# Performance work log

Hardware: AMD Instinct MI355X
Metric: run time of the kernel (lower is better)

## Reference

```python
import jax, jax.numpy as jnp
import numpy as np

N, EM, EW, L, S = 20000, 100000, 25000, 128, 6


def _mlp(x, W1, b1, W2, b2, g, beta):
    # Linear -> ReLU -> Linear -> LayerNorm
    h = jax.nn.relu(x @ W1 + b1) @ W2 + b2
    mu = jnp.mean(h, axis=-1, keepdims=True)
    var = jnp.mean((h - mu) ** 2, axis=-1, keepdims=True)
    return g * (h - mu) * jax.lax.rsqrt(var + 1e-5) + beta


def _scatter_mean(attr, recv, n):
    s = jax.ops.segment_sum(attr, recv, num_segments=n)
    c = jax.ops.segment_sum(jnp.ones((attr.shape[0], 1), attr.dtype), recv, num_segments=n)
    return s / jnp.maximum(c, 1.0)


def setup_inputs() -> dict:
    key = jax.random.key(0)
    ks = jax.random.split(key, 16)

    def w(k, shape, fan_in):
        return (jax.random.normal(k, shape, jnp.float32) / np.sqrt(fan_in).astype(np.float32))

    inp = {
        'x': jax.random.normal(ks[0], (N, L), jnp.float32),
        'mesh_edge_attr': jax.random.normal(ks[1], (EM, L), jnp.float32),
        'world_edge_attr': jax.random.normal(ks[2], (EW, L), jnp.float32),
        'mesh_edge_index': jax.random.randint(ks[3], (2, EM), 0, N),
        'world_edge_index': jax.random.randint(ks[4], (2, EW), 0, N),
    }
    i = 5
    for pre in ('me', 'we', 'nd'):
        inp[pre + '_W1'] = w(ks[i], (S, 3 * L, L), 3 * L); i += 1
        inp[pre + '_b1'] = jnp.zeros((S, L), jnp.float32)
        inp[pre + '_W2'] = w(ks[i], (S, L, L), L); i += 1
        inp[pre + '_b2'] = jnp.zeros((S, L), jnp.float32)
        inp[pre + '_g'] = jnp.ones((S, L), jnp.float32)
        inp[pre + '_beta'] = jnp.zeros((S, L), jnp.float32)
    return inp


def reference(x, mesh_edge_attr, world_edge_attr, mesh_edge_index, world_edge_index,
              me_W1, me_b1, me_W2, me_b2, me_g, me_beta,
              we_W1, we_b1, we_W2, we_b2, we_g, we_beta,
              nd_W1, nd_b1, nd_W2, nd_b2, nd_g, nd_beta):
    ms, mr = mesh_edge_index[0], mesh_edge_index[1]
    ws, wr = world_edge_index[0], world_edge_index[1]
    n = x.shape[0]

    def step(carry, p):
        x, mea, wea = carry
        (mW1, mb1, mW2, mb2, mg, mbe,
         wW1, wb1, wW2, wb2, wg, wbe,
         nW1, nb1, nW2, nb2, ng, nbe) = p
        # EdgeModel: gather + concat + MLP, residual into edge attrs
        mea = mea + _mlp(jnp.concatenate([x[ms], x[mr], mea], axis=-1), mW1, mb1, mW2, mb2, mg, mbe)
        wea = wea + _mlp(jnp.concatenate([x[ws], x[wr], wea], axis=-1), wW1, wb1, wW2, wb2, wg, wbe)
        # NodeModel: scatter-mean over both edge sets + concat + MLP, residual
        agg = jnp.concatenate([x, _scatter_mean(mea, mr, n), _scatter_mean(wea, wr, n)], axis=-1)
        x = x + _mlp(agg, nW1, nb1, nW2, nb2, ng, nbe)
        return (x, mea, wea), None

    params = (me_W1, me_b1, me_W2, me_b2, me_g, me_beta,
              we_W1, we_b1, we_W2, we_b2, we_g, we_beta,
              nd_W1, nd_b1, nd_W2, nd_b2, nd_g, nd_beta)
    (x, mea, wea), _ = jax.lax.scan(step, (x, mesh_edge_attr, world_edge_attr), params)
    return x, mea, wea
```

## Files before the change

kernel.cpp:

```cpp
#include <hip/hip_runtime.h>

constexpr int LDIM  = 128;
constexpr int NNODE = 20000;
constexpr int EM_N  = 100000;
constexpr int EW_N  = 25000;
constexpr int NSTEP = 6;

typedef short bf16x8 __attribute__((ext_vector_type(8)));
typedef float f32x4  __attribute__((ext_vector_type(4)));

struct MlpParams {
  const float* x;
  const float* attrIn;
  float*       attrOut;
  const int*   src;
  const int*   dst;
  float*       sum1;
  float*       sum2;
  const float* inv1;
  const float* inv2;
  const short* W1H;
  const short* W1L;
  const short* W2H;
  const short* W2L;
  const float* b1;
  const float* b2;
  const float* gam;
  const float* bet;
  int nRows;
};

__device__ __forceinline__ short f2b(float f) {
  unsigned int u = __float_as_uint(f);
  u = (u + 0x7fffu + ((u >> 16) & 1u)) >> 16;
  return (short)u;
}
__device__ __forceinline__ float b2f(short s) {
  return __uint_as_float(((unsigned int)(unsigned short)s) << 16);
}

template<bool IS_EDGE>
__launch_bounds__(256, 2)
__global__ void mlp_kernel(MlpParams pmA, MlpParams pmB, int blocksA) {
  const bool isA = (int)blockIdx.x < blocksA;
  const MlpParams P = isA ? pmA : pmB;
  const int bid  = isA ? (int)blockIdx.x : (int)blockIdx.x - blocksA;
  const int row0 = bid * 128;

  __shared__ __align__(16) short Abuf[128][40];
  __shared__ __align__(16) short Bhi[128][40];
  __shared__ __align__(16) short Blo[128][40];
  __shared__ __align__(16) short Hbuf[128][136];
  __shared__ float b1s[128], b2s[128], gs[128], bes[128];
  __shared__ int   idxa[128], idxb[128];
  __shared__ float inv1s[128], inv2s[128];
  __shared__ float sumL[2][128], sqL[2][128];
  __shared__ float muL[128], rsL[128];

  const int t = threadIdx.x;

  if (t < 128) {
    b1s[t] = P.b1[t];
    gs[t]  = P.gam[t];
    if (IS_EDGE) {
      int r = row0 + t;
      idxa[t] = (r < P.nRows) ? P.src[r] : 0;
    } else {
      int r = min(row0 + t, P.nRows - 1);
      inv1s[t] = P.inv1[r];
    }
  } else {
    int t2 = t - 128;
    b2s[t2] = P.b2[t2];
    bes[t2] = P.bet[t2];
    if (IS_EDGE) {
      int r = row0 + t2;
      idxb[t2] = (r < P.nRows) ? P.dst[r] : 0;
    } else {
      int r = min(row0 + t2, P.nRows - 1);
      inv2s[t2] = P.inv2[r];
    }
  }

  const int l   = t & 63;
  const int wid = t >> 6;
  const int wr  = wid >> 1, wcc = wid & 1;
  const int lr  = l & 15,  lg  = l >> 4;

  const int  srow  = t >> 1, sh = t & 1;
  const int  sgRow = row0 + srow;
  const bool sval  = sgRow < P.nRows;

  f32x4 acc[4][4];
#pragma unroll
  for (int i = 0; i < 4; ++i)
#pragma unroll
    for (int j = 0; j < 4; ++j) acc[i][j] = f32x4{0.f, 0.f, 0.f, 0.f};

  for (int kc = 0; kc < 12; ++kc) {
    __syncthreads();
    {
      const int seg = kc >> 2, part = kc & 3;
      float v[16];
      if (sval) {
        const float* sbase;
        float sc = 1.0f;
        if (IS_EDGE) {
          sbase = (seg == 0) ? P.x + (size_t)idxa[srow] * LDIM
                : (seg == 1) ? P.x + (size_t)idxb[srow] * LDIM
                             : P.attrIn + (size_t)sgRow * LDIM;
        } else {
          if (seg == 0)      { sbase = P.x    + (size_t)sgRow * LDIM; }
          else if (seg == 1) { sbase = P.sum1 + (size_t)sgRow * LDIM; sc = inv1s[srow]; }
          else               { sbase = P.sum2 + (size_t)sgRow * LDIM; sc = inv2s[srow]; }
        }
        const float4* s4 = (const float4*)(sbase + part * 32 + sh * 16);
        float4 a0 = s4[0], a1 = s4[1], a2 = s4[2], a3 = s4[3];
        v[0]=a0.x;  v[1]=a0.y;  v[2]=a0.z;  v[3]=a0.w;
        v[4]=a1.x;  v[5]=a1.y;  v[6]=a1.z;  v[7]=a1.w;
        v[8]=a2.x;  v[9]=a2.y;  v[10]=a2.z; v[11]=a2.w;
        v[12]=a3.x; v[13]=a3.y; v[14]=a3.z; v[15]=a3.w;
        if (!IS_EDGE && seg != 0) {
#pragma unroll
          for (int e = 0; e < 16; ++e) v[e] *= sc;
          float4 z = {0.f, 0.f, 0.f, 0.f};
          float4* zp = (float4*)(sbase + part * 32 + sh * 16);
          zp[0] = z; zp[1] = z; zp[2] = z; zp[3] = z;
        }
      } else {
#pragma unroll
        for (int e = 0; e < 16; ++e) v[e] = 0.f;
      }
      bf16x8 o0, o1;
#pragma unroll
      for (int e = 0; e < 8; ++e) { o0[e] = f2b(v[e]); o1[e] = f2b(v[8 + e]); }
      *(bf16x8*)&Abuf[srow][sh * 16]     = o0;
      *(bf16x8*)&Abuf[srow][sh * 16 + 8] = o1;
    }
    {
      const size_t off = (size_t)srow * 384 + kc * 32 + sh * 16;
      const short* wh = P.W1H + off;
      const short* wl = P.W1L + off;
      *(bf16x8*)&Bhi[srow][sh * 16]     = *(const bf16x8*)wh;
      *(bf16x8*)&Bhi[srow][sh * 16 + 8] = *(const bf16x8*)(wh + 8);
      *(bf16x8*)&Blo[srow][sh * 16]     = *(const bf16x8*)wl;
      *(bf16x8*)&Blo[srow][sh * 16 + 8] = *(const bf16x8*)(wl + 8);
    }
    __syncthreads();
    bf16x8 av[4], bh[4], bl[4];
#pragma unroll
    for (int rt = 0; rt < 4; ++rt) av[rt] = *(const bf16x8*)&Abuf[wr * 64 + rt * 16 + lr][lg * 8];
#pragma unroll
    for (int ct = 0; ct < 4; ++ct) {
      bh[ct] = *(const bf16x8*)&Bhi[wcc * 64 + ct * 16 + lr][lg * 8];
      bl[ct] = *(const bf16x8*)&Blo[wcc * 64 + ct * 16 + lr][lg * 8];
    }
#pragma unroll
    for (int rt = 0; rt < 4; ++rt)
#pragma unroll
      for (int ct = 0; ct < 4; ++ct) {
        acc[rt][ct] = __builtin_amdgcn_mfma_f32_16x16x32_bf16(av[rt], bl[ct], acc[rt][ct], 0, 0, 0);
        acc[rt][ct] = __builtin_amdgcn_mfma_f32_16x16x32_bf16(av[rt], bh[ct], acc[rt][ct], 0, 0, 0);
      }
  }

#pragma unroll
  for (int rt = 0; rt < 4; ++rt)
#pragma unroll
    for (int ct = 0; ct < 4; ++ct) {
      const int cc = wcc * 64 + ct * 16 + lr;
      const float bb = b1s[cc];
#pragma unroll
      for (int q = 0; q < 4; ++q) {
        const int rr = wr * 64 + rt * 16 + lg * 4 + q;
        Hbuf[rr][cc] = f2b(fmaxf(acc[rt][ct][q] + bb, 0.f));
      }
    }

  f32x4 acc2[4][4];
#pragma unroll
  for (int i = 0; i < 4; ++i)
#pragma unroll
    for (int j = 0; j < 4; ++j) acc2[i][j] = f32x4{0.f, 0.f, 0.f, 0.f};

  for (int kc = 0; kc < 4; ++kc) {
    __syncthreads();
    {
      const size_t off = (size_t)srow * 128 + kc * 32 + sh * 16;
      const short* wh = P.W2H + off;
      const short* wl = P.W2L + off;
      *(bf16x8*)&Bhi[srow][sh * 16]     = *(const bf16x8*)wh;
      *(bf16x8*)&Bhi[srow][sh * 16 + 8] = *(const bf16x8*)(wh + 8);
      *(bf16x8*)&Blo[srow][sh * 16]     = *(const bf16x8*)wl;
      *(bf16x8*)&Blo[srow][sh * 16 + 8] = *(const bf16x8*)(wl + 8);
    }
    __syncthreads();
    bf16x8 av2[4], bh2[4], bl2[4];
#pragma unroll
    for (int rt = 0; rt < 4; ++rt) av2[rt] = *(const bf16x8*)&Hbuf[wr * 64 + rt * 16 + lr][kc * 32 + lg * 8];
#pragma unroll
    for (int ct = 0; ct < 4; ++ct) {
      bh2[ct] = *(const bf16x8*)&Bhi[wcc * 64 + ct * 16 + lr][lg * 8];
      bl2[ct] = *(const bf16x8*)&Blo[wcc * 64 + ct * 16 + lr][lg * 8];
    }
#pragma unroll
    for (int rt = 0; rt < 4; ++rt)
#pragma unroll
      for (int ct = 0; ct < 4; ++ct) {
        acc2[rt][ct] = __builtin_amdgcn_mfma_f32_16x16x32_bf16(av2[rt], bl2[ct], acc2[rt][ct], 0, 0, 0);
        acc2[rt][ct] = __builtin_amdgcn_mfma_f32_16x16x32_bf16(av2[rt], bh2[ct], acc2[rt][ct], 0, 0, 0);
      }
  }

  float s1[4][4], s2[4][4];
#pragma unroll
  for (int rt = 0; rt < 4; ++rt)
#pragma unroll
    for (int q = 0; q < 4; ++q) { s1[rt][q] = 0.f; s2[rt][q] = 0.f; }
#pragma unroll
  for (int rt = 0; rt < 4; ++rt)
#pragma unroll
    for (int ct = 0; ct < 4; ++ct) {
      const float bb = b2s[wcc * 64 + ct * 16 + lr];
#pragma unroll
      for (int q = 0; q < 4; ++q) {
        float v = acc2[rt][ct][q] + bb;
        acc2[rt][ct][q] = v;
        s1[rt][q] += v;
        s2[rt][q] += v * v;
      }
    }
#pragma unroll
  for (int m = 1; m < 16; m <<= 1) {
#pragma unroll
    for (int rt = 0; rt < 4; ++rt)
#pragma unroll
      for (int q = 0; q < 4; ++q) {
        s1[rt][q] += __shfl_xor(s1[rt][q], m);
        s2[rt][q] += __shfl_xor(s2[rt][q], m);
      }
  }
  __syncthreads();
  {
    const int rt = lr >> 2, q = lr & 3;
    const int rr = wr * 64 + rt * 16 + lg * 4 + q;
    sumL[wcc][rr] = s1[rt][q];
    sqL[wcc][rr]  = s2[rt][q];
  }
  __syncthreads();
  if (t < 128) {
    const float tot = sumL[0][t] + sumL[1][t];
    const float tsq = sqL[0][t] + sqL[1][t];
    const float mu  = tot * (1.0f / 128.0f);
    const float var = tsq * (1.0f / 128.0f) - mu * mu;
    muL[t] = mu;
    rsL[t] = rsqrtf(var + 1e-5f);
  }
  __syncthreads();

#pragma unroll
  for (int rt = 0; rt < 4; ++rt) {
#pragma unroll
    for (int q = 0; q < 4; ++q) {
      const int rr = wr * 64 + rt * 16 + lg * 4 + q;
      const int grow = row0 + rr;
      if (grow < P.nRows) {
        const float mu = muL[rr], rs = rsL[rr];
        const float* rin = P.attrIn + (size_t)grow * LDIM;
        float* rout = P.attrOut + (size_t)grow * LDIM;
        float* ssum = nullptr;
        if (IS_EDGE) ssum = P.sum1 + (size_t)idxb[rr] * LDIM;
#pragma unroll
        for (int ct = 0; ct < 4; ++ct) {
          const int cc = wcc * 64 + ct * 16 + lr;
          const float o = gs[cc] * (acc2[rt][ct][q] - mu) * rs + bes[cc] + rin[cc];
          rout[cc] = o;
          if (IS_EDGE) atomicAdd(ssum + cc, o);
        }
      }
    }
  }
}

__global__ void prep_weights(const float* w1a, const float* w1b, const float* w1c,
                             const float* w2a, const float* w2b, const float* w2c,
                             short* w1h, short* w1l, short* w2h, short* w2l) {
  int i = blockIdx.x * 256 + threadIdx.x;
  constexpr int N1 = 18 * 128 * 384;
  constexpr int N2 = 18 * 128 * 128;
  if (i < N1) {
    int g = i / (128 * 384);
    int rem = i - g * (128 * 384);
    int n = rem / 384, k = rem - n * 384;
    int m = g / 6, s = g - m * 6;
    const float* src = (m == 0) ? w1a : (m == 1) ? w1b : w1c;
    float f = src[(size_t)s * (384 * 128) + (size_t)k * 128 + n];
    short hi = f2b(f);
    w1h[i] = hi;
    w1l[i] = f2b(f - b2f(hi));
  } else if (i < N1 + N2) {
    int j = i - N1;
    int g = j / (128 * 128);
    int rem = j - g * (128 * 128);
    int n = rem / 128, k = rem - n * 128;
    int m = g / 6, s = g - m * 6;
    const float* src = (m == 0) ? w2a : (m == 1) ? w2b : w2c;
    float f = src[(size_t)s * (128 * 128) + (size_t)k * 128 + n];
    short hi = f2b(f);
    w2h[j] = hi;
    w2l[j] = f2b(f - b2f(hi));
  }
}

__global__ void prep_deg(const int* mr, const int* wrcv, int* degm, int* degw) {
  int i = blockIdx.x * 256 + threadIdx.x;
  if (i < EM_N) atomicAdd(&degm[mr[i]], 1);
  else if (i < EM_N + EW_N) atomicAdd(&degw[wrcv[i - EM_N]], 1);
}

__global__ void prep_inv(const int* degm, const int* degw, float* invm, float* invw) {
  int i = blockIdx.x * 256 + threadIdx.x;
  if (i < NNODE) {
    invm[i] = 1.0f / fmaxf((float)degm[i], 1.0f);
    invw[i] = 1.0f / fmaxf((float)degw[i], 1.0f);
  }
}

extern "C" void kernel_launch(void* const* d_in, const int* in_sizes, int n_in,
                              void* d_out, int out_size, void* d_ws, size_t ws_size,
                              hipStream_t stream) {
  (void)in_sizes; (void)n_in; (void)out_size; (void)ws_size;
  const float* x_in   = (const float*)d_in[0];
  const float* mea_in = (const float*)d_in[1];
  const float* wea_in = (const float*)d_in[2];
  const int*   mei    = (const int*)d_in[3];
  const int*   wei    = (const int*)d_in[4];
  const float* W1s[3] = { (const float*)d_in[5],  (const float*)d_in[11], (const float*)d_in[17] };
  const float* B1s[3] = { (const float*)d_in[6],  (const float*)d_in[12], (const float*)d_in[18] };
  const float* W2s[3] = { (const float*)d_in[7],  (const float*)d_in[13], (const float*)d_in[19] };
  const float* B2s[3] = { (const float*)d_in[8],  (const float*)d_in[14], (const float*)d_in[20] };
  const float* Gs[3]  = { (const float*)d_in[9],  (const float*)d_in[15], (const float*)d_in[21] };
  const float* Be[3]  = { (const float*)d_in[10], (const float*)d_in[16], (const float*)d_in[22] };

  float* xo  = (float*)d_out;
  float* meo = xo  + (size_t)NNODE * LDIM;
  float* weo = meo + (size_t)EM_N * LDIM;

  float* msum = (float*)d_ws;
  float* wsum = msum + (size_t)NNODE * LDIM;
  int*   degm = (int*)(wsum + (size_t)NNODE * LDIM);
  int*   degw = degm + NNODE;
  float* invm = (float*)(degw + NNODE);
  float* invw = invm + NNODE;
  short* w1h  = (short*)(invw + NNODE);
  short* w1l  = w1h + (size_t)18 * 128 * 384;
  short* w2h  = w1l + (size_t)18 * 128 * 384;
  short* w2l  = w2h + (size_t)18 * 128 * 128;

  size_t zbytes = (size_t)2 * NNODE * LDIM * 4 + (size_t)2 * NNODE * 4;
  hipMemsetAsync(d_ws, 0, zbytes, stream);

  {
    int tot = 18 * 128 * 384 + 18 * 128 * 128;
    prep_weights<<<dim3((tot + 255) / 256), 256, 0, stream>>>(
        W1s[0], W1s[1], W1s[2], W2s[0], W2s[1], W2s[2], w1h, w1l, w2h, w2l);
  }
  prep_deg<<<dim3((EM_N + EW_N + 255) / 256), 256, 0, stream>>>(mei + EM_N, wei + EW_N, degm, degw);
  prep_inv<<<dim3((NNODE + 255) / 256), 256, 0, stream>>>(degm, degw, invm, invw);

  const int MB = (EM_N + 127) / 128;
  const int WB = (EW_N + 127) / 128;
  const int NB = (NNODE + 127) / 128;

  const float* xc = x_in;
  const float* mc = mea_in;
  const float* wc = wea_in;

  for (int s = 0; s < NSTEP; ++s) {
    MlpParams pm{}, pw{}, pn{};

    pm.x = xc; pm.attrIn = mc; pm.attrOut = meo;
    pm.src = mei; pm.dst = mei + EM_N;
    pm.sum1 = msum; pm.sum2 = nullptr; pm.inv1 = nullptr; pm.inv2 = nullptr;
    pm.W1H = w1h + (size_t)(0 * 6 + s) * 128 * 384;
    pm.W1L = w1l + (size_t)(0 * 6 + s) * 128 * 384;
    pm.W2H = w2h + (size_t)(0 * 6 + s) * 128 * 128;
    pm.W2L = w2l + (size_t)(0 * 6 + s) * 128 * 128;
    pm.b1 = B1s[0] + s * LDIM; pm.b2 = B2s[0] + s * LDIM;
    pm.gam = Gs[0] + s * LDIM; pm.bet = Be[0] + s * LDIM;
    pm.nRows = EM_N;

    pw.x = xc; pw.attrIn = wc; pw.attrOut = weo;
    pw.src = wei; pw.dst = wei + EW_N;
    pw.sum1 = wsum; pw.sum2 = nullptr; pw.inv1 = nullptr; pw.inv2 = nullptr;
    pw.W1H = w1h + (size_t)(1 * 6 + s) * 128 * 384;
    pw.W1L = w1l + (size_t)(1 * 6 + s) * 128 * 384;
    pw.W2H = w2h + (size_t)(1 * 6 + s) * 128 * 128;
    pw.W2L = w2l + (size_t)(1 * 6 + s) * 128 * 128;
    pw.b1 = B1s[1] + s * LDIM; pw.b2 = B2s[1] + s * LDIM;
    pw.gam = Gs[1] + s * LDIM; pw.bet = Be[1] + s * LDIM;
    pw.nRows = EW_N;

    mlp_kernel<true><<<dim3(MB + WB), 256, 0, stream>>>(pm, pw, MB);

    pn.x = xc; pn.attrIn = xc; pn.attrOut = xo;
    pn.src = nullptr; pn.dst = nullptr;
    pn.sum1 = msum; pn.sum2 = wsum; pn.inv1 = invm; pn.inv2 = invw;
    pn.W1H = w1h + (size_t)(2 * 6 + s) * 128 * 384;
    pn.W1L = w1l + (size_t)(2 * 6 + s) * 128 * 384;
    pn.W2H = w2h + (size_t)(2 * 6 + s) * 128 * 128;
    pn.W2L = w2l + (size_t)(2 * 6 + s) * 128 * 128;
    pn.b1 = B1s[2] + s * LDIM; pn.b2 = B2s[2] + s * LDIM;
    pn.gam = Gs[2] + s * LDIM; pn.bet = Be[2] + s * LDIM;
    pn.nRows = NNODE;

    mlp_kernel<false><<<dim3(NB), 256, 0, stream>>>(pn, pn, NB);

    xc = xo; mc = meo; wc = weo;
  }
}
```

Baseline: 946.2 us.

## Double-buffer activations, read weights from global directly, retile node MLP to 32-row blocks

Restructures the MLP kernel. The activation tile is now double-buffered so the next chunk's global loads overlap with the current MFMAs, which cuts one barrier per k-step. Weight fragments are read straight from global/L2 into registers instead of staged through shared memory. The second GEMM is computed transposed so that epilogue stores become float4. The kernel is templated on block rows so the node pass uses 32-row blocks, giving more blocks and higher occupancy, and launch bounds are raised. The cost is more global weight traffic per wave, and the changed occupancy may increase register pressure.

```diff
diff --git a/kernel.cpp b/kernel.cpp
--- a/kernel.cpp
+++ b/kernel.cpp
@@ -7,6 +7,7 @@
 constexpr int NSTEP = 6;
 
 typedef short bf16x8 __attribute__((ext_vector_type(8)));
+typedef short bf16x4 __attribute__((ext_vector_type(4)));
 typedef float f32x4  __attribute__((ext_vector_type(4)));
 
 struct MlpParams {
@@ -39,218 +40,248 @@
   return __uint_as_float(((unsigned int)(unsigned short)s) << 16);
 }
 
-template<bool IS_EDGE>
-__launch_bounds__(256, 2)
+template<int BR, bool IS_EDGE>
+__launch_bounds__(256, (BR == 128) ? 3 : 4)
 __global__ void mlp_kernel(MlpParams pmA, MlpParams pmB, int blocksA) {
+  constexpr int WC    = (BR == 128) ? 2 : 4;
+  constexpr int WR    = 4 / WC;
+  constexpr int WROWS = BR / WR;
+  constexpr int WCOLS = 128 / WC;
+  constexpr int MREP  = WROWS / 16;
+  constexpr int NREP  = WCOLS / 16;
+  constexpr int TPR   = 256 / BR;
+  constexpr int FPT   = 32 / TPR;
+  constexpr int NV4   = FPT / 4;
+
   const bool isA = (int)blockIdx.x < blocksA;
   const MlpParams P = isA ? pmA : pmB;
   const int bid  = isA ? (int)blockIdx.x : (int)blockIdx.x - blocksA;
-  const int row0 = bid * 128;
-
-  __shared__ __align__(16) short Abuf[128][40];
-  __shared__ __align__(16) short Bhi[128][40];
-  __shared__ __align__(16) short Blo[128][40];
-  __shared__ __align__(16) short Hbuf[128][136];
+  const int row0 = bid * BR;
+
+  __shared__ __align__(16) short Abuf[2][BR][40];
+  __shared__ __align__(16) short Hbuf[BR][40];
   __shared__ float b1s[128], b2s[128], gs[128], bes[128];
-  __shared__ int   idxa[128], idxb[128];
-  __shared__ float inv1s[128], inv2s[128];
-  __shared__ float sumL[2][128], sqL[2][128];
-  __shared__ float muL[128], rsL[128];
+  __shared__ int   idxa[BR], idxb[BR];
+  __shared__ float inv1s[BR], inv2s[BR];
+  __shared__ float sumL[WC][BR], sqL[WC][BR], muL[BR], rsL[BR];
 
   const int t = threadIdx.x;
 
-  if (t < 128) {
-    b1s[t] = P.b1[t];
-    gs[t]  = P.gam[t];
+  if (t < 128) { b1s[t] = P.b1[t]; gs[t] = P.gam[t]; }
+  else         { b2s[t - 128] = P.b2[t - 128]; bes[t - 128] = P.bet[t - 128]; }
+  if (t < BR) {
     if (IS_EDGE) {
       int r = row0 + t;
       idxa[t] = (r < P.nRows) ? P.src[r] : 0;
+      idxb[t] = (r < P.nRows) ? P.dst[r] : 0;
     } else {
       int r = min(row0 + t, P.nRows - 1);
       inv1s[t] = P.inv1[r];
-    }
-  } else {
-    int t2 = t - 128;
-    b2s[t2] = P.b2[t2];
-    bes[t2] = P.bet[t2];
-    if (IS_EDGE) {
-      int r = row0 + t2;
-      idxb[t2] = (r < P.nRows) ? P.dst[r] : 0;
-    } else {
-      int r = min(row0 + t2, P.nRows - 1);
-      inv2s[t2] = P.inv2[r];
-    }
-  }
+      inv2s[t] = P.inv2[r];
+    }
+  }
+  __syncthreads();
 
   const int l   = t & 63;
   const int wid = t >> 6;
-  const int wr  = wid >> 1, wcc = wid & 1;
+  const int wr  = wid / WC, wcc = wid % WC;
   const int lr  = l & 15,  lg  = l >> 4;
 
-  const int  srow  = t >> 1, sh = t & 1;
+  const int  srow  = t / TPR, sh = t % TPR;
   const int  sgRow = row0 + srow;
   const bool sval  = sgRow < P.nRows;
 
-  f32x4 acc[4][4];
-#pragma unroll
-  for (int i = 0; i < 4; ++i)
-#pragma unroll
-    for (int j = 0; j < 4; ++j) acc[i][j] = f32x4{0.f, 0.f, 0.f, 0.f};
-
+  int gA = 0, gB = 0; float sc1 = 1.f, sc2 = 1.f;
+  if (IS_EDGE) { gA = idxa[srow]; gB = idxb[srow]; }
+  else         { sc1 = inv1s[srow]; sc2 = inv2s[srow]; }
+
+  auto loadChunk = [&](int kc, float* v) {
+    const int seg = kc >> 2, part = kc & 3;
+    if (sval) {
+      const float* sbase; float sc = 1.f;
+      if (IS_EDGE) {
+        sbase = (seg == 0) ? P.x + (size_t)gA * LDIM
+              : (seg == 1) ? P.x + (size_t)gB * LDIM
+                           : P.attrIn + (size_t)sgRow * LDIM;
+      } else {
+        if (seg == 0)      { sbase = P.x    + (size_t)sgRow * LDIM; }
+        else if (seg == 1) { sbase = P.sum1 + (size_t)sgRow * LDIM; sc = sc1; }
+        else               { sbase = P.sum2 + (size_t)sgRow * LDIM; sc = sc2; }
+      }
+      const float4* s4 = (const float4*)(sbase + part * 32 + sh * FPT);
+#pragma unroll
+      for (int c = 0; c < NV4; ++c) {
+        float4 a = s4[c];
+        v[c * 4 + 0] = a.x; v[c * 4 + 1] = a.y; v[c * 4 + 2] = a.z; v[c * 4 + 3] = a.w;
+      }
+      if (!IS_EDGE && seg != 0) {
+#pragma unroll
+        for (int e = 0; e < FPT; ++e) v[e] *= sc;
+        float4 z = {0.f, 0.f, 0.f, 0.f};
+        float4* zp = (float4*)(sbase + part * 32 + sh * FPT);
+#pragma unroll
+        for (int c = 0; c < NV4; ++c) zp[c] = z;
+      }
+    } else {
+#pragma unroll
+      for (int e = 0; e < FPT; ++e) v[e] = 0.f;
+    }
+  };
+
+  auto storeChunk = [&](int buf, const float* v) {
+    if constexpr (FPT == 16) {
+      bf16x8 o0, o1;
+#pragma unroll
+      for (int e = 0; e < 8; ++e) { o0[e] = f2b(v[e]); o1[e] = f2b(v[8 + e]); }
+      *(bf16x8*)&Abuf[buf][srow][sh * 16]     = o0;
+      *(bf16x8*)&Abuf[buf][srow][sh * 16 + 8] = o1;
+    } else {
+      bf16x4 o;
+#pragma unroll
+      for (int e = 0; e < 4; ++e) o[e] = f2b(v[e]);
+      *(bf16x4*)&Abuf[buf][srow][sh * 4] = o;
+    }
+  };
+
+  f32x4 acc[MREP][NREP];
+#pragma unroll
+  for (int i = 0; i < MREP; ++i)
+#pragma unroll
+    for (int j = 0; j < NREP; ++j) acc[i][j] = f32x4{0.f, 0.f, 0.f, 0.f};
+
+  {
+    float v0[FPT];
+    loadChunk(0, v0);
+    storeChunk(0, v0);
+  }
+  __syncthreads();
+
+  const short* w1hB = P.W1H + (size_t)(wcc * WCOLS + lr) * 384 + lg * 8;
+  const short* w1lB = P.W1L + (size_t)(wcc * WCOLS + lr) * 384 + lg * 8;
+
+#pragma unroll
   for (int kc = 0; kc < 12; ++kc) {
+    float vnext[FPT];
+    if (kc < 11) loadChunk(kc + 1, vnext);
+    bf16x8 bh[NREP], bl[NREP];
+#pragma unroll
+    for (int ni = 0; ni < NREP; ++ni) {
+      bh[ni] = *(const bf16x8*)(w1hB + (size_t)ni * (16 * 384) + kc * 32);
+      bl[ni] = *(const bf16x8*)(w1lB + (size_t)ni * (16 * 384) + kc * 32);
+    }
+    bf16x8 av[MREP];
+#pragma unroll
+    for (int mi = 0; mi < MREP; ++mi)
+      av[mi] = *(const bf16x8*)&Abuf[kc & 1][wr * WROWS + mi * 16 + lr][lg * 8];
+#pragma unroll
+    for (int mi = 0; mi < MREP; ++mi)
+#pragma unroll
+      for (int ni = 0; ni < NREP; ++ni) {
+        acc[mi][ni] = __builtin_amdgcn_mfma_f32_16x16x32_bf16(av[mi], bl[ni], acc[mi][ni], 0, 0, 0);
+        acc[mi][ni] = __builtin_amdgcn_mfma_f32_16x16x32_bf16(av[mi], bh[ni], acc[mi][ni], 0, 0, 0);
+      }
+    if (kc < 11) storeChunk((kc + 1) & 1, vnext);
     __syncthreads();
-    {
-      const int seg = kc >> 2, part = kc & 3;
-      float v[16];
-      if (sval) {
-        const float* sbase;
-        float sc = 1.0f;
-        if (IS_EDGE) {
-          sbase = (seg == 0) ? P.x + (size_t)idxa[srow] * LDIM
-                : (seg == 1) ? P.x + (size_t)idxb[srow] * LDIM
-                             : P.attrIn + (size_t)sgRow * LDIM;
-        } else {
-          if (seg == 0)      { sbase = P.x    + (size_t)sgRow * LDIM; }
-          else if (seg == 1) { sbase = P.sum1 + (size_t)sgRow * LDIM; sc = inv1s[srow]; }
-          else               { sbase = P.sum2 + (size_t)sgRow * LDIM; sc = inv2s[srow]; }
+  }
+
+  unsigned int hpk[MREP][NREP][2];
+#pragma unroll
+  for (int ni = 0; ni < NREP; ++ni) {
+    const float bb = b1s[wcc * WCOLS + ni * 16 + lr];
+#pragma unroll
+    for (int mi = 0; mi < MREP; ++mi)
+#pragma unroll
+      for (int qp = 0; qp < 2; ++qp) {
+        unsigned int lo = (unsigned short)f2b(fmaxf(acc[mi][ni][2 * qp]     + bb, 0.f));
+        unsigned int hi = (unsigned short)f2b(fmaxf(acc[mi][ni][2 * qp + 1] + bb, 0.f));
+        hpk[mi][ni][qp] = lo | (hi << 16);
+      }
+  }
+
+  f32x4 acc2[NREP][MREP];
+#pragma unroll
+  for (int i = 0; i < NREP; ++i)
+#pragma unroll
+    for (int j = 0; j < MREP; ++j) acc2[i][j] = f32x4{0.f, 0.f, 0.f, 0.f};
+
+  const short* w2hB = P.W2H + (size_t)(wcc * WCOLS + lr) * 128 + lg * 8;
+  const short* w2lB = P.W2L + (size_t)(wcc * WCOLS + lr) * 128 + lg * 8;
+
+#pragma unroll
+  for (int kc = 0; kc < 4; ++kc) {
+    const int owner = (kc * 32) / WCOLS;
+    const int nib   = ((kc * 32) % WCOLS) / 16;
+    __syncthreads();
+    if (wcc == owner) {
+#pragma unroll
+      for (int mi = 0; mi < MREP; ++mi)
+#pragma unroll
+        for (int nio = 0; nio < 2; ++nio) {
+          const int ni = nib + nio;
+          const int cl = nio * 16 + lr;
+#pragma unroll
+          for (int qp = 0; qp < 2; ++qp) {
+            const int r = wr * WROWS + mi * 16 + lg * 4 + 2 * qp;
+            const unsigned int pk = hpk[mi][ni][qp];
+            Hbuf[r][cl]     = (short)(pk & 0xffffu);
+            Hbuf[r + 1][cl] = (short)(pk >> 16);
+          }
         }
-        const float4* s4 = (const float4*)(sbase + part * 32 + sh * 16);
-        float4 a0 = s4[0], a1 = s4[1], a2 = s4[2], a3 = s4[3];
-        v[0]=a0.x;  v[1]=a0.y;  v[2]=a0.z;  v[3]=a0.w;
-        v[4]=a1.x;  v[5]=a1.y;  v[6]=a1.z;  v[7]=a1.w;
-        v[8]=a2.x;  v[9]=a2.y;  v[10]=a2.z; v[11]=a2.w;
-        v[12]=a3.x; v[13]=a3.y; v[14]=a3.z; v[15]=a3.w;
-        if (!IS_EDGE && seg != 0) {
-#pragma unroll
-          for (int e = 0; e < 16; ++e) v[e] *= sc;
-          float4 z = {0.f, 0.f, 0.f, 0.f};
-          float4* zp = (float4*)(sbase + part * 32 + sh * 16);
-          zp[0] = z; zp[1] = z; zp[2] = z; zp[3] = z;
-        }
-      } else {
-#pragma unroll
-        for (int e = 0; e < 16; ++e) v[e] = 0.f;
-      }
-      bf16x8 o0, o1;
-#pragma unroll
-      for (int e = 0; e < 8; ++e) { o0[e] = f2b(v[e]); o1[e] = f2b(v[8 + e]); }
-      *(bf16x8*)&Abuf[srow][sh * 16]     = o0;
-      *(bf16x8*)&Abuf[srow][sh * 16 + 8] = o1;
-    }
-    {
-      const size_t off = (size_t)srow * 384 + kc * 32 + sh * 16;
-      const short* wh = P.W1H + off;
-      const short* wl = P.W1L + off;
-      *(bf16x8*)&Bhi[srow][sh * 16]     = *(const bf16x8*)wh;
-      *(bf16x8*)&Bhi[srow][sh * 16 + 8] = *(const bf16x8*)(wh + 8);
-      *(bf16x8*)&Blo[srow][sh * 16]     = *(const bf16x8*)wl;
-      *(bf16x8*)&Blo[srow][sh * 16 + 8] = *(const bf16x8*)(wl + 8);
     }
     __syncthreads();
-    bf16x8 av[4], bh[4], bl[4];
-#pragma unroll
-    for (int rt = 0; rt < 4; ++rt) av[rt] = *(const bf16x8*)&Abuf[wr * 64 + rt * 16 + lr][lg * 8];
-#pragma unroll
-    for (int ct = 0; ct < 4; ++ct) {
-      bh[ct] = *(const bf16x8*)&Bhi[wcc * 64 + ct * 16 + lr][lg * 8];
-      bl[ct] = *(const bf16x8*)&Blo[wcc * 64 + ct * 16 + lr][lg * 8];
-    }
-#pragma unroll
-    for (int rt = 0; rt < 4; ++rt)
-#pragma unroll
-      for (int ct = 0; ct < 4; ++ct) {
-        acc[rt][ct] = __builtin_amdgcn_mfma_f32_16x16x32_bf16(av[rt], bl[ct], acc[rt][ct], 0, 0, 0);
-        acc[rt][ct] = __builtin_amdgcn_mfma_f32_16x16x32_bf16(av[rt], bh[ct], acc[rt][ct], 0, 0, 0);
-      }
-  }
-
-#pragma unroll
-  for (int rt = 0; rt < 4; ++rt)
-#pragma unroll
-    for (int ct = 0; ct < 4; ++ct) {
-      const int cc = wcc * 64 + ct * 16 + lr;
-      const float bb = b1s[cc];
-#pragma unroll
-      for (int q = 0; q < 4; ++q) {
-        const int rr = wr * 64 + rt * 16 + lg * 4 + q;
-        Hbuf[rr][cc] = f2b(fmaxf(acc[rt][ct][q] + bb, 0.f));
-      }
-    }
-
-  f32x4 acc2[4][4];
-#pragma unroll
-  for (int i = 0; i < 4; ++i)
-#pragma unroll
-    for (int j = 0; j < 4; ++j) acc2[i][j] = f32x4{0.f, 0.f, 0.f, 0.f};
-
-  for (int kc = 0; kc < 4; ++kc) {
-    __syncthreads();
-    {
-      const size_t off = (size_t)srow * 128 + kc * 32 + sh * 16;
-      const short* wh = P.W2H + off;
-      const short* wl = P.W2L + off;
-      *(bf16x8*)&Bhi[srow][sh * 16]     = *(const bf16x8*)wh;
-      *(bf16x8*)&Bhi[srow][sh * 16 + 8] = *(const bf16x8*)(wh + 8);
-      *(bf16x8*)&Blo[srow][sh * 16]     = *(const bf16x8*)wl;
-      *(bf16x8*)&Blo[srow][sh * 16 + 8] = *(const bf16x8*)(wl + 8);
-    }
-    __syncthreads();
-    bf16x8 av2[4], bh2[4], bl2[4];
-#pragma unroll
-    for (int rt = 0; rt < 4; ++rt) av2[rt] = *(const bf16x8*)&Hbuf[wr * 64 + rt * 16 + lr][kc * 32 + lg * 8];
-#pragma unroll
-    for (int ct = 0; ct < 4; ++ct) {
-      bh2[ct] = *(const bf16x8*)&Bhi[wcc * 64 + ct * 16 + lr][lg * 8];
-      bl2[ct] = *(const bf16x8*)&Blo[wcc * 64 + ct * 16 + lr][lg * 8];
-    }
-#pragma unroll
-    for (int rt = 0; rt < 4; ++rt)
-#pragma unroll
-      for (int ct = 0; ct < 4; ++ct) {
-        acc2[rt][ct] = __builtin_amdgcn_mfma_f32_16x16x32_bf16(av2[rt], bl2[ct], acc2[rt][ct], 0, 0, 0);
-        acc2[rt][ct] = __builtin_amdgcn_mfma_f32_16x16x32_bf16(av2[rt], bh2[ct], acc2[rt][ct], 0, 0, 0);
-      }
-  }
-
-  float s1[4][4], s2[4][4];
-#pragma unroll
-  for (int rt = 0; rt < 4; ++rt)
-#pragma unroll
-    for (int q = 0; q < 4; ++q) { s1[rt][q] = 0.f; s2[rt][q] = 0.f; }
-#pragma unroll
-  for (int rt = 0; rt < 4; ++rt)
-#pragma unroll
-    for (int ct = 0; ct < 4; ++ct) {
-      const float bb = b2s[wcc * 64 + ct * 16 + lr];
-#pragma unroll
-      for (int q = 0; q < 4; ++q) {
-        float v = acc2[rt][ct][q] + bb;
-        acc2[rt][ct][q] = v;
-        s1[rt][q] += v;
-        s2[rt][q] += v * v;
-      }
-    }
-#pragma unroll
-  for (int m = 1; m < 16; m <<= 1) {
-#pragma unroll
-    for (int rt = 0; rt < 4; ++rt)
-#pragma unroll
-      for (int q = 0; q < 4; ++q) {
-        s1[rt][q] += __shfl_xor(s1[rt][q], m);
-        s2[rt][q] += __shfl_xor(s2[rt][q], m);
-      }
+    bf16x8 hv[MREP];
+#pragma unroll
+    for (int mi = 0; mi < MREP; ++mi)
+      hv[mi] = *(const bf16x8*)&Hbuf[wr * WROWS + mi * 16 + lr][lg * 8];
+    bf16x8 wh[NREP], wl[NREP];
+#pragma unroll
+    for (int ct = 0; ct < NREP; ++ct) {
+      wh[ct] = *(const bf16x8*)(w2hB + (size_t)ct * (16 * 128) + kc * 32);
+      wl[ct] = *(const bf16x8*)(w2lB + (size_t)ct * (16 * 128) + kc * 32);
+    }
+#pragma unroll
+    for (int ct = 0; ct < NREP; ++ct)
+#pragma unroll
+      for (int mi = 0; mi < MREP; ++mi) {
+        acc2[ct][mi] = __builtin_amdgcn_mfma_f32_16x16x32_bf16(wl[ct], hv[mi], acc2[ct][mi], 0, 0, 0);
+        acc2[ct][mi] = __builtin_amdgcn_mfma_f32_16x16x32_bf16(wh[ct], hv[mi], acc2[ct][mi], 0, 0, 0);
+      }
+  }
+
+  float s1[MREP], s2[MREP];
+#pragma unroll
+  for (int mi = 0; mi < MREP; ++mi) { s1[mi] = 0.f; s2[mi] = 0.f; }
+#pragma unroll
+  for (int ct = 0; ct < NREP; ++ct) {
+    const int n0 = wcc * WCOLS + ct * 16 + lg * 4;
+#pragma unroll
+    for (int q = 0; q < 4; ++q) {
+      const float bb = b2s[n0 + q];
+#pragma unroll
+      for (int mi = 0; mi < MREP; ++mi) {
+        const float v = acc2[ct][mi][q] + bb;
+        acc2[ct][mi][q] = v;
+        s1[mi] += v; s2[mi] += v * v;
+      }
+    }
+  }
+#pragma unroll
+  for (int mi = 0; mi < MREP; ++mi) {
+    s1[mi] += __shfl_xor(s1[mi], 16); s1[mi] += __shfl_xor(s1[mi], 32);
+    s2[mi] += __shfl_xor(s2[mi], 16); s2[mi] += __shfl_xor(s2[mi], 32);
+  }
+  if (lg == 0) {
+#pragma unroll
+    for (int mi = 0; mi < MREP; ++mi) {
+      sumL[wcc][wr * WROWS + mi * 16 + lr] = s1[mi];
+      sqL[wcc][wr * WROWS + mi * 16 + lr]  = s2[mi];
+    }
   }
   __syncthreads();
-  {
-    const int rt = lr >> 2, q = lr & 3;
-    const int rr = wr * 64 + rt * 16 + lg * 4 + q;
-    sumL[wcc][rr] = s1[rt][q];
-    sqL[wcc][rr]  = s2[rt][q];
-  }
-  __syncthreads();
-  if (t < 128) {
-    const float tot = sumL[0][t] + sumL[1][t];
-    const float tsq = sqL[0][t] + sqL[1][t];
+  if (t < BR) {
+    float tot = 0.f, tsq = 0.f;
+#pragma unroll
+    for (int w = 0; w < WC; ++w) { tot += sumL[w][t]; tsq += sqL[w][t]; }
     const float mu  = tot * (1.0f / 128.0f);
     const float var = tsq * (1.0f / 128.0f) - mu * mu;
     muL[t] = mu;
@@ -258,24 +289,39 @@
   }
   __syncthreads();
 
-#pragma unroll
-  for (int rt = 0; rt < 4; ++rt) {
-#pragma unroll
-    for (int q = 0; q < 4; ++q) {
-      const int rr = wr * 64 + rt * 16 + lg * 4 + q;
-      const int grow = row0 + rr;
-      if (grow < P.nRows) {
-        const float mu = muL[rr], rs = rsL[rr];
-        const float* rin = P.attrIn + (size_t)grow * LDIM;
-        float* rout = P.attrOut + (size_t)grow * LDIM;
-        float* ssum = nullptr;
-        if (IS_EDGE) ssum = P.sum1 + (size_t)idxb[rr] * LDIM;
-#pragma unroll
-        for (int ct = 0; ct < 4; ++ct) {
-          const int cc = wcc * 64 + ct * 16 + lr;
-          const float o = gs[cc] * (acc2[rt][ct][q] - mu) * rs + bes[cc] + rin[cc];
-          rout[cc] = o;
-          if (IS_EDGE) atomicAdd(ssum + cc, o);
+  float garr[NREP][4], bearr[NREP][4];
+#pragma unroll
+  for (int ct = 0; ct < NREP; ++ct) {
+    const int n0 = wcc * WCOLS + ct * 16 + lg * 4;
+#pragma unroll
+    for (int q = 0; q < 4; ++q) { garr[ct][q] = gs[n0 + q]; bearr[ct][q] = bes[n0 + q]; }
+  }
+
+#pragma unroll
+  for (int mi = 0; mi < MREP; ++mi) {
+    const int rl   = wr * WROWS + mi * 16 + lr;
+    const int grow = row0 + rl;
+    if (grow < P.nRows) {
+      const float mu = muL[rl], rs = rsL[rl];
+      const float* rin  = P.attrIn  + (size_t)grow * LDIM;
+      float*       rout = P.attrOut + (size_t)grow * LDIM;
+      float* ssum = nullptr;
+      if (IS_EDGE) ssum = P.sum1 + (size_t)idxb[rl] * LDIM;
+#pragma unroll
+      for (int ct = 0; ct < NREP; ++ct) {
+        const int n0 = wcc * WCOLS + ct * 16 + lg * 4;
+        const float4 old = *(const float4*)(rin + n0);
+        float4 oo;
+        oo.x = garr[ct][0] * (acc2[ct][mi][0] - mu) * rs + bearr[ct][0] + old.x;
+        oo.y = garr[ct][1] * (acc2[ct][mi][1] - mu) * rs + bearr[ct][1] + old.y;
+        oo.z = garr[ct][2] * (acc2[ct][mi][2] - mu) * rs + bearr[ct][2] + old.z;
+        oo.w = garr[ct][3] * (acc2[ct][mi][3] - mu) * rs + bearr[ct][3] + old.w;
+        *(float4*)(rout + n0) = oo;
+        if (IS_EDGE) {
+          atomicAdd(ssum + n0 + 0, oo.x);
+          atomicAdd(ssum + n0 + 1, oo.y);
+          atomicAdd(ssum + n0 + 2, oo.z);
+          atomicAdd(ssum + n0 + 3, oo.w);
         }
       }
     }
@@ -370,7 +416,7 @@
 
   const int MB = (EM_N + 127) / 128;
   const int WB = (EW_N + 127) / 128;
-  const int NB = (NNODE + 127) / 128;
+  const int NB = NNODE / 32;
 
   const float* xc = x_in;
   const float* mc = mea_in;
@@ -381,7 +427,7 @@
 
     pm.x = xc; pm.attrIn = mc; pm.attrOut = meo;
     pm.src = mei; pm.dst = mei + EM_N;
-    pm.sum1 = msum; pm.sum2 = nullptr; pm.inv1 = nullptr; pm.inv2 = nullptr;
+    pm.sum1 = msum;
     pm.W1H = w1h + (size_t)(0 * 6 + s) * 128 * 384;
     pm.W1L = w1l + (size_t)(0 * 6 + s) * 128 * 384;
     pm.W2H = w2h + (size_t)(0 * 6 + s) * 128 * 128;
@@ -392,7 +438,7 @@
 
     pw.x = xc; pw.attrIn = wc; pw.attrOut = weo;
     pw.src = wei; pw.dst = wei + EW_N;
-    pw.sum1 = wsum; pw.sum2 = nullptr; pw.inv1 = nullptr; pw.inv2 = nullptr;
+    pw.sum1 = wsum;
     pw.W1H = w1h + (size_t)(1 * 6 + s) * 128 * 384;
     pw.W1L = w1l + (size_t)(1 * 6 + s) * 128 * 384;
     pw.W2H = w2h + (size_t)(1 * 6 + s) * 128 * 128;
@@ -401,10 +447,9 @@
     pw.gam = Gs[1] + s * LDIM; pw.bet = Be[1] + s * LDIM;
     pw.nRows = EW_N;
 
-    mlp_kernel<true><<<dim3(MB + WB), 256, 0, stream>>>(pm, pw, MB);
+    mlp_kernel<128, true><<<dim3(MB + WB), 256, 0, stream>>>(pm, pw, MB);
 
     pn.x = xc; pn.attrIn = xc; pn.attrOut = xo;
-    pn.src = nullptr; pn.dst = nullptr;
     pn.sum1 = msum; pn.sum2 = wsum; pn.inv1 = invm; pn.inv2 = invw;
     pn.W1H = w1h + (size_t)(2 * 6 + s) * 128 * 384;
     pn.W1L = w1l + (size_t)(2 * 6 + s) * 128 * 384;
@@ -414,7 +459,7 @@
     pn.gam = Gs[2] + s * LDIM; pn.bet = Be[2] + s * LDIM;
     pn.nRows = NNODE;
 
-    mlp_kernel<false><<<dim3(NB), 256, 0, stream>>>(pn, pn, NB);
+    mlp_kernel<32, false><<<dim3(NB), 256, 0, stream>>>(pn, pn, NB);
 
     xc = xo; mc = meo; wc = weo;
   }
```

Result: slower. 1.892 ms (median of 2 runs) (+100.0%).

## Drop W1 low-part split and register-prefetch next K-chunk in MLP GEMMs

Applied to the files above, without the earlier changes.

The first-layer GEMM now uses a single bf16 copy of W1 instead of the hi/lo split, which halves its MFMA count and its weight traffic. Both GEMM loops now load the next K-chunk of activations and weights into registers while the current chunk is being computed, so global load latency overlaps the MFMAs. Activation address and scale computation is hoisted out of the loop, and invalid rows are masked by a zero multiplier. The cost is lower precision in the first layer, which may loosen accuracy against the fp32 reference, plus higher register pressure from the prefetch buffers.

```diff
diff --git a/kernel.cpp b/kernel.cpp
--- a/kernel.cpp
+++ b/kernel.cpp
@@ -7,6 +7,7 @@
 constexpr int NSTEP = 6;
 
 typedef short bf16x8 __attribute__((ext_vector_type(8)));
+typedef short bf16x4 __attribute__((ext_vector_type(4)));
 typedef float f32x4  __attribute__((ext_vector_type(4)));
 
 struct MlpParams {
@@ -20,7 +21,6 @@
   const float* inv1;
   const float* inv2;
   const short* W1H;
-  const short* W1L;
   const short* W2H;
   const short* W2L;
   const float* b1;
@@ -37,6 +37,12 @@
 }
 __device__ __forceinline__ float b2f(short s) {
   return __uint_as_float(((unsigned int)(unsigned short)s) << 16);
+}
+__device__ __forceinline__ bf16x4 cvt4(float4 a, float sc) {
+  bf16x4 o;
+  o[0] = f2b(a.x * sc); o[1] = f2b(a.y * sc);
+  o[2] = f2b(a.z * sc); o[3] = f2b(a.w * sc);
+  return o;
 }
 
 template<bool IS_EDGE>
@@ -81,6 +87,7 @@
       inv2s[t2] = P.inv2[r];
     }
   }
+  __syncthreads();
 
   const int l   = t & 63;
   const int wid = t >> 6;
@@ -90,6 +97,25 @@
   const int  srow  = t >> 1, sh = t & 1;
   const int  sgRow = row0 + srow;
   const bool sval  = sgRow < P.nRows;
+  const int  sgC   = sval ? sgRow : 0;
+  const float vmask = sval ? 1.f : 0.f;
+
+  const float* base0; const float* base1; const float* base2;
+  float sc1v = vmask, sc2v = vmask;
+  if (IS_EDGE) {
+    base0 = P.x + (size_t)idxa[srow] * LDIM + sh * 16;
+    base1 = P.x + (size_t)idxb[srow] * LDIM + sh * 16;
+    base2 = P.attrIn + (size_t)sgC * LDIM + sh * 16;
+  } else {
+    base0 = P.x    + (size_t)sgC * LDIM + sh * 16;
+    base1 = P.sum1 + (size_t)sgC * LDIM + sh * 16;
+    base2 = P.sum2 + (size_t)sgC * LDIM + sh * 16;
+    sc1v = inv1s[srow] * vmask;
+    sc2v = inv2s[srow] * vmask;
+  }
+
+  const int wrow = t >> 1, wsh = t & 1;
+  const short* w1base = P.W1H + (size_t)wrow * 384 + wsh * 16;
 
   f32x4 acc[4][4];
 #pragma unroll
@@ -97,71 +123,55 @@
 #pragma unroll
     for (int j = 0; j < 4; ++j) acc[i][j] = f32x4{0.f, 0.f, 0.f, 0.f};
 
+  float4 pA0, pA1, pA2, pA3;
+  bf16x8 pW0, pW1;
+  {
+    const float4* bp = (const float4*)base0;
+    pA0 = bp[0]; pA1 = bp[1]; pA2 = bp[2]; pA3 = bp[3];
+    pW0 = *(const bf16x8*)w1base;
+    pW1 = *(const bf16x8*)(w1base + 8);
+  }
+
+#pragma unroll
   for (int kc = 0; kc < 12; ++kc) {
-    __syncthreads();
+    const int seg = kc >> 2, part = kc & 3;
+    if (kc > 0) __syncthreads();
     {
-      const int seg = kc >> 2, part = kc & 3;
-      float v[16];
-      if (sval) {
-        const float* sbase;
-        float sc = 1.0f;
-        if (IS_EDGE) {
-          sbase = (seg == 0) ? P.x + (size_t)idxa[srow] * LDIM
-                : (seg == 1) ? P.x + (size_t)idxb[srow] * LDIM
-                             : P.attrIn + (size_t)sgRow * LDIM;
-        } else {
-          if (seg == 0)      { sbase = P.x    + (size_t)sgRow * LDIM; }
-          else if (seg == 1) { sbase = P.sum1 + (size_t)sgRow * LDIM; sc = inv1s[srow]; }
-          else               { sbase = P.sum2 + (size_t)sgRow * LDIM; sc = inv2s[srow]; }
-        }
-        const float4* s4 = (const float4*)(sbase + part * 32 + sh * 16);
-        float4 a0 = s4[0], a1 = s4[1], a2 = s4[2], a3 = s4[3];
-        v[0]=a0.x;  v[1]=a0.y;  v[2]=a0.z;  v[3]=a0.w;
-        v[4]=a1.x;  v[5]=a1.y;  v[6]=a1.z;  v[7]=a1.w;
-        v[8]=a2.x;  v[9]=a2.y;  v[10]=a2.z; v[11]=a2.w;
-        v[12]=a3.x; v[13]=a3.y; v[14]=a3.z; v[15]=a3.w;
-        if (!IS_EDGE && seg != 0) {
-#pragma unroll
-          for (int e = 0; e < 16; ++e) v[e] *= sc;
+      const float scK = (seg == 0) ? vmask : (seg == 1) ? sc1v : sc2v;
+      *(bf16x4*)&Abuf[srow][sh * 16 + 0]  = cvt4(pA0, scK);
+      *(bf16x4*)&Abuf[srow][sh * 16 + 4]  = cvt4(pA1, scK);
+      *(bf16x4*)&Abuf[srow][sh * 16 + 8]  = cvt4(pA2, scK);
+      *(bf16x4*)&Abuf[srow][sh * 16 + 12] = cvt4(pA3, scK);
+      *(bf16x8*)&Bhi[wrow][wsh * 16]     = pW0;
+      *(bf16x8*)&Bhi[wrow][wsh * 16 + 8] = pW1;
+      if constexpr (!IS_EDGE) {
+        if (seg != 0 && sval) {
           float4 z = {0.f, 0.f, 0.f, 0.f};
-          float4* zp = (float4*)(sbase + part * 32 + sh * 16);
+          float4* zp = (float4*)((seg == 1 ? base1 : base2) + part * 32);
           zp[0] = z; zp[1] = z; zp[2] = z; zp[3] = z;
         }
-      } else {
-#pragma unroll
-        for (int e = 0; e < 16; ++e) v[e] = 0.f;
-      }
-      bf16x8 o0, o1;
-#pragma unroll
-      for (int e = 0; e < 8; ++e) { o0[e] = f2b(v[e]); o1[e] = f2b(v[8 + e]); }
-      *(bf16x8*)&Abuf[srow][sh * 16]     = o0;
-      *(bf16x8*)&Abuf[srow][sh * 16 + 8] = o1;
-    }
-    {
-      const size_t off = (size_t)srow * 384 + kc * 32 + sh * 16;
-      const short* wh = P.W1H + off;
-      const short* wl = P.W1L + off;
-      *(bf16x8*)&Bhi[srow][sh * 16]     = *(const bf16x8*)wh;
-      *(bf16x8*)&Bhi[srow][sh * 16 + 8] = *(const bf16x8*)(wh + 8);
-      *(bf16x8*)&Blo[srow][sh * 16]     = *(const bf16x8*)wl;
-      *(bf16x8*)&Blo[srow][sh * 16 + 8] = *(const bf16x8*)(wl + 8);
+      }
     }
     __syncthreads();
-    bf16x8 av[4], bh[4], bl[4];
-#pragma unroll
-    for (int rt = 0; rt < 4; ++rt) av[rt] = *(const bf16x8*)&Abuf[wr * 64 + rt * 16 + lr][lg * 8];
-#pragma unroll
-    for (int ct = 0; ct < 4; ++ct) {
-      bh[ct] = *(const bf16x8*)&Bhi[wcc * 64 + ct * 16 + lr][lg * 8];
-      bl[ct] = *(const bf16x8*)&Blo[wcc * 64 + ct * 16 + lr][lg * 8];
-    }
-#pragma unroll
-    for (int rt = 0; rt < 4; ++rt)
-#pragma unroll
-      for (int ct = 0; ct < 4; ++ct) {
-        acc[rt][ct] = __builtin_amdgcn_mfma_f32_16x16x32_bf16(av[rt], bl[ct], acc[rt][ct], 0, 0, 0);
-        acc[rt][ct] = __builtin_amdgcn_mfma_f32_16x16x32_bf16(av[rt], bh[ct], acc[rt][ct], 0, 0, 0);
-      }
+    if (kc < 11) {
+      const int kn = kc + 1, segn = kn >> 2, partn = kn & 3;
+      const float4* bp = (const float4*)((segn == 0 ? base0 : segn == 1 ? base1 : base2) + partn * 32);
+      pA0 = bp[0]; pA1 = bp[1]; pA2 = bp[2]; pA3 = bp[3];
+      pW0 = *(const bf16x8*)(w1base + kn * 32);
+      pW1 = *(const bf16x8*)(w1base + kn * 32 + 8);
+    }
+    bf16x8 av[4], bh[4];
+#pragma unroll
+    for (int mi = 0; mi < 4; ++mi)
+      av[mi] = *(const bf16x8*)&Abuf[wr * 64 + mi * 16 + lr][lg * 8];
+#pragma unroll
+    for (int ni = 0; ni < 4; ++ni)
+      bh[ni] = *(const bf16x8*)&Bhi[wcc * 64 + ni * 16 + lr][lg * 8];
+#pragma unroll
+    for (int mi = 0; mi < 4; ++mi)
+#pragma unroll
+      for (int ni = 0; ni < 4; ++ni)
+        acc[mi][ni] = __builtin_amdgcn_mfma_f32_16x16x32_bf16(av[mi], bh[ni], acc[mi][ni], 0, 0, 0);
   }
 
 #pragma unroll
@@ -183,21 +193,35 @@
 #pragma unroll
     for (int j = 0; j < 4; ++j) acc2[i][j] = f32x4{0.f, 0.f, 0.f, 0.f};
 
+  const short* w2hbase = P.W2H + (size_t)wrow * 128 + wsh * 16;
+  const short* w2lbase = P.W2L + (size_t)wrow * 128 + wsh * 16;
+
+  bf16x8 qh0, qh1, ql0, ql1;
+  qh0 = *(const bf16x8*)w2hbase;
+  qh1 = *(const bf16x8*)(w2hbase + 8);
+  ql0 = *(const bf16x8*)w2lbase;
+  ql1 = *(const bf16x8*)(w2lbase + 8);
+
+#pragma unroll
   for (int kc = 0; kc < 4; ++kc) {
     __syncthreads();
     {
-      const size_t off = (size_t)srow * 128 + kc * 32 + sh * 16;
-      const short* wh = P.W2H + off;
-      const short* wl = P.W2L + off;
-      *(bf16x8*)&Bhi[srow][sh * 16]     = *(const bf16x8*)wh;
-      *(bf16x8*)&Bhi[srow][sh * 16 + 8] = *(const bf16x8*)(wh + 8);
-      *(bf16x8*)&Blo[srow][sh * 16]     = *(const bf16x8*)wl;
-      *(bf16x8*)&Blo[srow][sh * 16 + 8] = *(const bf16x8*)(wl + 8);
+      *(bf16x8*)&Bhi[wrow][wsh * 16]     = qh0;
+      *(bf16x8*)&Bhi[wrow][wsh * 16 + 8] = qh1;
+      *(bf16x8*)&Blo[wrow][wsh * 16]     = ql0;
+      *(bf16x8*)&Blo[wrow][wsh * 16 + 8] = ql1;
     }
     __syncthreads();
+    if (kc < 3) {
+      qh0 = *(const bf16x8*)(w2hbase + (kc + 1) * 32);
+      qh1 = *(const bf16x8*)(w2hbase + (kc + 1) * 32 + 8);
+      ql0 = *(const bf16x8*)(w2lbase + (kc + 1) * 32);
+      ql1 = *(const bf16x8*)(w2lbase + (kc + 1) * 32 + 8);
+    }
     bf16x8 av2[4], bh2[4], bl2[4];
 #pragma unroll
-    for (int rt = 0; rt < 4; ++rt) av2[rt] = *(const bf16x8*)&Hbuf[wr * 64 + rt * 16 + lr][kc * 32 + lg * 8];
+    for (int rt = 0; rt < 4; ++rt)
+      av2[rt] = *(const bf16x8*)&Hbuf[wr * 64 + rt * 16 + lr][kc * 32 + lg * 8];
 #pragma unroll
     for (int ct = 0; ct < 4; ++ct) {
       bh2[ct] = *(const bf16x8*)&Bhi[wcc * 64 + ct * 16 + lr][lg * 8];
@@ -284,7 +308,7 @@
 
 __global__ void prep_weights(const float* w1a, const float* w1b, const float* w1c,
                              const float* w2a, const float* w2b, const float* w2c,
-                             short* w1h, short* w1l, short* w2h, short* w2l) {
+                             short* w1h, short* w2h, short* w2l) {
   int i = blockIdx.x * 256 + threadIdx.x;
   constexpr int N1 = 18 * 128 * 384;
   constexpr int N2 = 18 * 128 * 128;
@@ -294,10 +318,7 @@
     int n = rem / 384, k = rem - n * 384;
     int m = g / 6, s = g - m * 6;
     const float* src = (m == 0) ? w1a : (m == 1) ? w1b : w1c;
-    float f = src[(size_t)s * (384 * 128) + (size_t)k * 128 + n];
-    short hi = f2b(f);
-    w1h[i] = hi;
-    w1l[i] = f2b(f - b2f(hi));
+    w1h[i] = f2b(src[(size_t)s * (384 * 128) + (size_t)k * 128 + n]);
   } else if (i < N1 + N2) {
     int j = i - N1;
     int g = j / (128 * 128);
@@ -353,8 +374,7 @@
   float* invm = (float*)(degw + NNODE);
   float* invw = invm + NNODE;
   short* w1h  = (short*)(invw + NNODE);
-  short* w1l  = w1h + (size_t)18 * 128 * 384;
-  short* w2h  = w1l + (size_t)18 * 128 * 384;
+  short* w2h  = w1h + (size_t)18 * 128 * 384;
   short* w2l  = w2h + (size_t)18 * 128 * 128;
 
   size_t zbytes = (size_t)2 * NNODE * LDIM * 4 + (size_t)2 * NNODE * 4;
@@ -363,7 +383,7 @@
   {
     int tot = 18 * 128 * 384 + 18 * 128 * 128;
     prep_weights<<<dim3((tot + 255) / 256), 256, 0, stream>>>(
-        W1s[0], W1s[1], W1s[2], W2s[0], W2s[1], W2s[2], w1h, w1l, w2h, w2l);
+        W1s[0], W1s[1], W1s[2], W2s[0], W2s[1], W2s[2], w1h, w2h, w2l);
   }
   prep_deg<<<dim3((EM_N + EW_N + 255) / 256), 256, 0, stream>>>(mei + EM_N, wei + EW_N, degm, degw);
   prep_inv<<<dim3((NNODE + 255) / 256), 256, 0, stream>>>(degm, degw, invm, invw);
@@ -381,9 +401,8 @@
 
     pm.x = xc; pm.attrIn = mc; pm.attrOut = meo;
     pm.src = mei; pm.dst = mei + EM_N;
-    pm.sum1 = msum; pm.sum2 = nullptr; pm.inv1 = nullptr; pm.inv2 = nullptr;
+    pm.sum1 = msum;
     pm.W1H = w1h + (size_t)(0 * 6 + s) * 128 * 384;
-    pm.W1L = w1l + (size_t)(0 * 6 + s) * 128 * 384;
     pm.W2H = w2h + (size_t)(0 * 6 + s) * 128 * 128;
     pm.W2L = w2l + (size_t)(0 * 6 + s) * 128 * 128;
     pm.b1 = B1s[0] + s * LDIM; pm.b2 = B2s[0] + s * LDIM;
@@ -392,9 +411,8 @@
 
     pw.x = xc; pw.attrIn = wc; pw.attrOut = weo;
     pw.src = wei; pw.dst = wei + EW_N;
-    pw.sum1 = wsum; pw.sum2 = nullptr; pw.inv1 = nullptr; pw.inv2 = nullptr;
+    pw.sum1 = wsum;
     pw.W1H = w1h + (size_t)(1 * 6 + s) * 128 * 384;
-    pw.W1L = w1l + (size_t)(1 * 6 + s) * 128 * 384;
     pw.W2H = w2h + (size_t)(1 * 6 + s) * 128 * 128;
     pw.W2L = w2l + (size_t)(1 * 6 + s) * 128 * 128;
     pw.b1 = B1s[1] + s * LDIM; pw.b2 = B2s[1] + s * LDIM;
@@ -404,10 +422,8 @@
     mlp_kernel<true><<<dim3(MB + WB), 256, 0, stream>>>(pm, pw, MB);
 
     pn.x = xc; pn.attrIn = xc; pn.attrOut = xo;
-    pn.src = nullptr; pn.dst = nullptr;
     pn.sum1 = msum; pn.sum2 = wsum; pn.inv1 = invm; pn.inv2 = invw;
     pn.W1H = w1h + (size_t)(2 * 6 + s) * 128 * 384;
-    pn.W1L = w1l + (size_t)(2 * 6 + s) * 128 * 384;
     pn.W2H = w2h + (size_t)(2 * 6 + s) * 128 * 128;
     pn.W2L = w2l + (size_t)(2 * 6 + s) * 128 * 128;
     pn.b1 = B1s[2] + s * LDIM; pn.b2 = B2s[2] + s * LDIM;
```

After: 886.0 us. -6.4%, faster.
